# Performance work log

Measured on AMD Instinct MI355X. Metric: run time of the kernel, lower is better.

Reference implementation:

```python
import jax, jax.numpy as jnp
import numpy as np

NP_, NT_, NA_, NG_ = 50000, 200000, 20000, 500
ED, HID, H, C, L = 64, 64, 4, 16, 2
NEG_SLOPE = 0.2


def _edges(key, e, ns, nd):
    k1, k2 = jax.random.split(key)
    return jnp.stack([jax.random.randint(k1, (e,), 0, ns, dtype=jnp.int32),
                      jax.random.randint(k2, (e,), 0, nd, dtype=jnp.int32)])


def setup_inputs() -> dict:
    key = jax.random.key(0)
    ks = iter(jax.random.split(key, 64))
    nrm = lambda shp, s=0.1: (jax.random.normal(next(ks), shp, jnp.float32) * s)
    inp = {
        'playlist_x': nrm((NP_, 8), 1.0), 'track_x': nrm((NT_, 7), 1.0),
        'artist_x': nrm((NA_, 1), 1.0), 'genre_x': nrm((NG_, NG_), 1.0),
        'emb_playlist': nrm((NP_, ED)), 'emb_artist': nrm((NA_, ED)),
        'pf_W': nrm((8, ED)), 'pf_b': jnp.zeros((ED,)),
        'tf_W': nrm((7, ED)), 'tf_b': jnp.zeros((ED,)),
        'af_W': nrm((1, ED)), 'af_b': jnp.zeros((ED,)),
        'gf_W': nrm((NG_, ED)), 'gf_b': jnp.zeros((ED,)),
        'ip_W_playlist': nrm((2 * ED, HID)), 'ip_b_playlist': jnp.zeros((HID,)),
        'ip_W_track': nrm((ED, HID)), 'ip_b_track': jnp.zeros((HID,)),
        'ip_W_artist': nrm((2 * ED, HID)), 'ip_b_artist': jnp.zeros((HID,)),
        'ip_W_genre': nrm((ED, HID)), 'ip_b_genre': jnp.zeros((HID,)),
        # 8 relations x L layers, shared lin per relation (PyG GATConv with int in_channels)
        'gat_W': nrm((L, 8, HID, H * C)), 'gat_b': jnp.zeros((L, 8, H * C)),
        'gat_as': nrm((L, 8, H, C)), 'gat_ad': nrm((L, 8, H, C)),
        'ln_w': jnp.ones((L, HID)), 'ln_b': jnp.zeros((L, HID)),
        'op_W_playlist': nrm((HID, ED)), 'op_b_playlist': jnp.zeros((ED,)),
        'op_W_track': nrm((HID, ED)), 'op_b_track': jnp.zeros((ED,)),
        'op_W_artist': nrm((HID, ED)), 'op_b_artist': jnp.zeros((ED,)),
        'op_W_genre': nrm((HID, ED)), 'op_b_genre': jnp.zeros((ED,)),
        'playlist_idx': jnp.arange(NP_, dtype=jnp.int32),
        'artist_idx': jnp.arange(NA_, dtype=jnp.int32),
        'ei_contains': _edges(next(ks), 1000000, NP_, NT_),
        'ei_in_playlist': _edges(next(ks), 1000000, NT_, NP_),
        'ei_by': _edges(next(ks), 200000, NT_, NA_),
        'ei_created': _edges(next(ks), 200000, NA_, NT_),
        'ei_has_genre': _edges(next(ks), 600000, NT_, NG_),
        'ei_includes': _edges(next(ks), 600000, NG_, NT_),
        'ei_performs': _edges(next(ks), 60000, NA_, NG_),
        'ei_performed_by': _edges(next(ks), 60000, NG_, NA_),
    }
    return inp


def _gat(x_src, x_dst, ei, W, b, a_s, a_d, n_dst):
    # PyG GATConv: shared lin, edge softmax over dst, scatter-add aggregation
    hs = (x_src @ W).reshape(x_src.shape[0], H, C)
    hd = (x_dst @ W).reshape(x_dst.shape[0], H, C)
    es, ed = ei[0], ei[1]
    al_s = jnp.einsum('nhc,hc->nh', hs, a_s)  # [Ns,H]
    al_d = jnp.einsum('nhc,hc->nh', hd, a_d)  # [Nd,H]
    alpha = jax.nn.leaky_relu(al_s[es] + al_d[ed], NEG_SLOPE)  # [E,H]
    amax = jax.ops.segment_max(alpha, ed, num_segments=n_dst)
    amax = jnp.where(jnp.isfinite(amax), amax, 0.0)
    ex = jnp.exp(alpha - amax[ed])
    den = jax.ops.segment_sum(ex, ed, num_segments=n_dst)
    coef = ex / (den[ed] + 1e-16)
    msg = (hs[es] * coef[:, :, None]).reshape(es.shape[0], H * C)  # [E,H*C]
    return jax.ops.segment_sum(msg, ed, num_segments=n_dst) + b


def _ln(x, w, b):
    m = jnp.mean(x, -1, keepdims=True)
    v = jnp.mean((x - m) ** 2, -1, keepdims=True)
    return (x - m) * jax.lax.rsqrt(v + 1e-5) * w + b


def _forward(playlist_x, track_x, artist_x, genre_x, emb_playlist, emb_artist,
             pf_W, pf_b, tf_W, tf_b, af_W, af_b, gf_W, gf_b,
             ip_W_playlist, ip_b_playlist, ip_W_track, ip_b_track,
             ip_W_artist, ip_b_artist, ip_W_genre, ip_b_genre,
             gat_W, gat_b, gat_as, gat_ad, ln_w, ln_b,
             op_W_playlist, op_b_playlist, op_W_track, op_b_track,
             op_W_artist, op_b_artist, op_W_genre, op_b_genre,
             playlist_idx, artist_idx, ei_contains, ei_in_playlist, ei_by,
             ei_created, ei_has_genre, ei_includes, ei_performs, ei_performed_by):
    h_p = jnp.concatenate([emb_playlist[playlist_idx], playlist_x @ pf_W + pf_b], -1) @ ip_W_playlist + ip_b_playlist
    h_t = (track_x @ tf_W + tf_b) @ ip_W_track + ip_b_track
    h_a = jnp.concatenate([emb_artist[artist_idx], artist_x @ af_W + af_b], -1) @ ip_W_artist + ip_b_artist
    h_g = (genre_x @ gf_W + gf_b) @ ip_W_genre + ip_b_genre
    for i in range(L):
        pp, pt, pa, pg = h_p, h_t, h_a, h_g
        g = lambda r, xs, xd, ei, nd: _gat(xs, xd, ei, gat_W[i, r], gat_b[i, r], gat_as[i, r], gat_ad[i, r], nd)
        # relation index: 0 contains,1 in_playlist,2 by,3 created,4 has_genre,5 includes_track,6 performs_genre,7 performed_by
        nt = g(0, pp, pt, ei_contains, NT_) + g(3, pa, pt, ei_created, NT_) + g(5, pg, pt, ei_includes, NT_)
        np2 = g(1, pt, pp, ei_in_playlist, NP_)
        na = g(2, pt, pa, ei_by, NA_) + g(7, pg, pa, ei_performed_by, NA_)
        ng = g(4, pt, pg, ei_has_genre, NG_) + g(6, pa, pg, ei_performs, NG_)
        h_p, h_t, h_a, h_g = jax.nn.relu(np2), jax.nn.relu(nt), jax.nn.relu(na), jax.nn.relu(ng)
        if i > 0:  # residual only after first layer (matches `if i > 0`)
            h_p, h_t, h_a, h_g = h_p + pp, h_t + pt, h_a + pa, h_g + pg
        h_p, h_t, h_a, h_g = (_ln(v, ln_w[i], ln_b[i]) for v in (h_p, h_t, h_a, h_g))
    return jnp.concatenate([
        h_p @ op_W_playlist + op_b_playlist,
        h_t @ op_W_track + op_b_track,
        h_a @ op_W_artist + op_b_artist,
        h_g @ op_W_genre + op_b_genre], axis=0)  # [NP+NT+NA+NG, 64]


def reference(playlist_x, track_x, artist_x, genre_x, emb_playlist, emb_artist,
              pf_W, pf_b, tf_W, tf_b, af_W, af_b, gf_W, gf_b,
              ip_W_playlist, ip_b_playlist, ip_W_track, ip_b_track,
              ip_W_artist, ip_b_artist, ip_W_genre, ip_b_genre,
              gat_W, gat_b, gat_as, gat_ad, ln_w, ln_b,
              op_W_playlist, op_b_playlist, op_W_track, op_b_track,
              op_W_artist, op_b_artist, op_W_genre, op_b_genre,
              playlist_idx, artist_idx, ei_contains, ei_in_playlist, ei_by,
              ei_created, ei_has_genre, ei_includes, ei_performs, ei_performed_by):
    return _forward(playlist_x, track_x, artist_x, genre_x, emb_playlist, emb_artist,
                    pf_W, pf_b, tf_W, tf_b, af_W, af_b, gf_W, gf_b,
                    ip_W_playlist, ip_b_playlist, ip_W_track, ip_b_track,
                    ip_W_artist, ip_b_artist, ip_W_genre, ip_b_genre,
                    gat_W, gat_b, gat_as, gat_ad, ln_w, ln_b,
                    op_W_playlist, op_b_playlist, op_W_track, op_b_track,
                    op_W_artist, op_b_artist, op_W_genre, op_b_genre,
                    playlist_idx, artist_idx, ei_contains, ei_in_playlist, ei_by,
                    ei_created, ei_has_genre, ei_includes, ei_performs, ei_performed_by)
```

## Files before the change

### kernel.cpp

```cpp
#include <hip/hip_runtime.h>
#include <cstdint>

constexpr int NP=50000, NT=200000, NA=20000, NG=500;
constexpr int NTOT = NP+NT+NA+NG;
constexpr int RO_P=0, RO_T=NP, RO_A=NP+NT, RO_G=NP+NT+NA;
constexpr int E_TOT = 3720000;

constexpr int H_E [8] = {1000000,1000000,200000,200000,600000,600000,60000,60000};
constexpr int H_ES[9] = {0,1000000,2000000,2200000,2400000,3000000,3600000,3660000,3720000};
constexpr int H_NS[8] = {NP,NT,NT,NA,NT,NG,NA,NG};
constexpr int H_ND[8] = {NT,NP,NA,NT,NG,NT,NG,NA};
constexpr int H_SO[8] = {RO_P,RO_T,RO_T,RO_A,RO_T,RO_G,RO_A,RO_G};
constexpr int H_DO[8] = {RO_T,RO_P,RO_A,RO_T,RO_G,RO_T,RO_G,RO_A};
constexpr int H_RPO[8]= {0,200001,250002,270003,470004,470505,670506,671007};
constexpr int H_CO[8] = {0,200000,250000,270000,470000,470500,670500,671000};

__constant__ int c_E [8] = {1000000,1000000,200000,200000,600000,600000,60000,60000};
__constant__ int c_ES[9] = {0,1000000,2000000,2200000,2400000,3000000,3600000,3660000,3720000};
__constant__ int c_ND[8] = {200000,50000,20000,200000,500,200000,500,20000};
__constant__ int c_RPO[8]= {0,200001,250002,270003,470004,470505,670506,671007};
__constant__ int c_CO[8] = {0,200000,250000,270000,470000,470500,670500,671000};

__constant__ int sb_pref[9] = {0,196,245,265,461,462,658,659,679};
constexpr int SB_BLOCKS = 679;

constexpr int WSZ = 16384;
__constant__ int c_G [8] = {8,8,2,2,5,5,1,1};
__constant__ int c_CS[8] = {125000,125000,100000,100000,120000,120000,60000,60000};
__constant__ int c_NW[8] = {13,4,2,13,1,13,1,2};
__constant__ int gw_pref[9] = {0,104,136,140,166,171,236,237,239};
constexpr int GW_BLOCKS = 239;
__constant__ int c_C2[8] = {0,1600000,2000000,2040000,2440000,2442500,3442500,3443000};

constexpr int OWT=0;
constexpr int OBT=448;
constexpr int OWPX=512;
constexpr int OBP=1024;
constexpr int OAV=1088;
constexpr int OBA=1152;
constexpr int OBG=1216;
constexpr int OBAGG=1280;
constexpr int OWAS=1792;
constexpr int OWAD=5888;
constexpr int OWG=9984;

struct EiPtrs { const int* p[8]; };

__global__ __launch_bounds__(256) void k_prep(
  const float* __restrict__ pf_W, const float* __restrict__ pf_b,
  const float* __restrict__ tf_W, const float* __restrict__ tf_b,
  const float* __restrict__ af_W, const float* __restrict__ af_b,
  const float* __restrict__ gf_W, const float* __restrict__ gf_b,
  const float* __restrict__ ipWp, const float* __restrict__ ipbp,
  const float* __restrict__ ipWt, const float* __restrict__ ipbt,
  const float* __restrict__ ipWa, const float* __restrict__ ipba,
  const float* __restrict__ ipWg, const float* __restrict__ ipbg,
  const float* __restrict__ gatW, const float* __restrict__ gatB,
  const float* __restrict__ gatAs, const float* __restrict__ gatAd,
  float* __restrict__ cb)
{
  int tid = blockIdx.x*256 + threadIdx.x;
  int STR = gridDim.x*256;
  for(int i=tid;i<7*64;i+=STR){ int j=i>>6,c=i&63; float s=0.f;
    for(int k=0;k<64;k++) s += tf_W[j*64+k]*ipWt[k*64+c];
    cb[OWT+i]=s; }
  for(int i=tid;i<64;i+=STR){ float s=ipbt[i];
    for(int k=0;k<64;k++) s += tf_b[k]*ipWt[k*64+i];
    cb[OBT+i]=s; }
  for(int i=tid;i<8*64;i+=STR){ int j=i>>6,c=i&63; float s=0.f;
    for(int k=0;k<64;k++) s += pf_W[j*64+k]*ipWp[(64+k)*64+c];
    cb[OWPX+i]=s; }
  for(int i=tid;i<64;i+=STR){ float s=ipbp[i];
    for(int k=0;k<64;k++) s += pf_b[k]*ipWp[(64+k)*64+i];
    cb[OBP+i]=s; }
  for(int i=tid;i<64;i+=STR){ float s=0.f;
    for(int k=0;k<64;k++) s += af_W[k]*ipWa[(64+k)*64+i];
    cb[OAV+i]=s; }
  for(int i=tid;i<64;i+=STR){ float s=ipba[i];
    for(int k=0;k<64;k++) s += af_b[k]*ipWa[(64+k)*64+i];
    cb[OBA+i]=s; }
  for(int i=tid;i<64;i+=STR){ float s=ipbg[i];
    for(int k=0;k<64;k++) s += gf_b[k]*ipWg[k*64+i];
    cb[OBG+i]=s; }
  for(int i=tid;i<512;i+=STR){ int l=i>>8, t=(i>>6)&3, c=i&63;
    const float* B = gatB + l*8*64; float s;
    if(t==0)      s = B[1*64+c];
    else if(t==1) s = B[0*64+c]+B[3*64+c]+B[5*64+c];
    else if(t==2) s = B[2*64+c]+B[7*64+c];
    else          s = B[4*64+c]+B[6*64+c];
    cb[OBAGG+i]=s; }
  for(int i=tid;i<2*8*64*4;i+=STR){ int h=i&3, k=(i>>2)&63, lr=i>>8;
    const float* as = gatAs + lr*64;
    cb[OWAS+i] = ((k>>4)==h) ? as[h*16 + (k&15)] : 0.f;
    const float* W  = gatW + (size_t)lr*4096;
    const float* ad = gatAd + lr*64 + h*16;
    float d=0.f;
    for(int c=0;c<16;c++){ d += W[k*64+h*16+c]*ad[c]; }
    cb[OWAD+i]=d; }
  for(int i=tid;i<512*64;i+=STR){ int g=i>>6,c=i&63; float s=0.f;
    if(g<500){ for(int k=0;k<64;k++) s += gf_W[g*64+k]*ipWg[k*64+c]; }
    cb[OWG+i]=s; }
}

#define MM_DECL  __shared__ float sX[64*65]; __shared__ float sW[64*68]; \
  int tid=threadIdx.x; int rt=(tid>>4)<<2, ct=(tid&15)<<2; float acc[4][4];

#define MM_LOOP() \
  _Pragma("unroll 8") \
  for(int k=0;k<64;k++){ \
    float4 wv = *(const float4*)&sW[k*68+ct]; \
    float x0=sX[(rt+0)*65+k], x1=sX[(rt+1)*65+k], x2=sX[(rt+2)*65+k], x3=sX[(rt+3)*65+k]; \
    acc[0][0]+=x0*wv.x; acc[0][1]+=x0*wv.y; acc[0][2]+=x0*wv.z; acc[0][3]+=x0*wv.w; \
    acc[1][0]+=x1*wv.x; acc[1][1]+=x1*wv.y; acc[1][2]+=x1*wv.z; acc[1][3]+=x1*wv.w; \
    acc[2][0]+=x2*wv.x; acc[2][1]+=x2*wv.y; acc[2][2]+=x2*wv.z; acc[2][3]+=x2*wv.w; \
    acc[3][0]+=x3*wv.x; acc[3][1]+=x3*wv.y; acc[3][2]+=x3*wv.z; acc[3][3]+=x3*wv.w; \
  }

template<bool ALS>
__global__ __launch_bounds__(256) void k_mm64(const float* __restrict__ X, const float* __restrict__ W,
  const float* __restrict__ bias, float* __restrict__ Y, float* __restrict__ alsY,
  const float* __restrict__ was, int N)
{
  MM_DECL
  int row0 = blockIdx.x*64;
  for(int i=tid;i<4096;i+=256){
    int r=i>>6, k=i&63;
    sX[r*65+k] = (row0+r<N)? X[(size_t)(row0+r)*64+k] : 0.f;
    sW[r*68+k] = W[i];
  }
  __syncthreads();
  #pragma unroll
  for(int i=0;i<4;i++){ acc[i][0]=0.f;acc[i][1]=0.f;acc[i][2]=0.f;acc[i][3]=0.f; }
  MM_LOOP()
  float4 bv = make_float4(0.f,0.f,0.f,0.f);
  if(bias) bv = *(const float4*)&bias[ct];
  #pragma unroll
  for(int i=0;i<4;i++){
    int row=row0+rt+i;
    if(row<N) *(float4*)&Y[(size_t)row*64+ct] =
      make_float4(acc[i][0]+bv.x, acc[i][1]+bv.y, acc[i][2]+bv.z, acc[i][3]+bv.w);
  }
  if(ALS){
    float4 w0 = *(const float4*)&was[(ct+0)*4];
    float4 w1 = *(const float4*)&was[(ct+1)*4];
    float4 w2 = *(const float4*)&was[(ct+2)*4];
    float4 w3 = *(const float4*)&was[(ct+3)*4];
    #pragma unroll
    for(int i=0;i<4;i++){
      float4 p;
      p.x = acc[i][0]*w0.x + acc[i][1]*w1.x + acc[i][2]*w2.x + acc[i][3]*w3.x;
      p.y = acc[i][0]*w0.y + acc[i][1]*w1.y + acc[i][2]*w2.y + acc[i][3]*w3.y;
      p.z = acc[i][0]*w0.z + acc[i][1]*w1.z + acc[i][2]*w2.z + acc[i][3]*w3.z;
      p.w = acc[i][0]*w0.w + acc[i][1]*w1.w + acc[i][2]*w2.w + acc[i][3]*w3.w;
      #pragma unroll
      for(int m=1;m<16;m<<=1){
        p.x+=__shfl_xor(p.x,m); p.y+=__shfl_xor(p.y,m);
        p.z+=__shfl_xor(p.z,m); p.w+=__shfl_xor(p.w,m);
      }
      int row=row0+rt+i;
      if((tid&15)==0 && row<N) *(float4*)&alsY[(size_t)row*4] = p;
    }
  }
}

constexpr int BP=(NP+63)/64, BT=(NT+63)/64, BA=(NA+63)/64;
__global__ __launch_bounds__(256) void k_init(
  const float* __restrict__ px, const float* __restrict__ tx, const float* __restrict__ ax,
  const float* __restrict__ embp, const float* __restrict__ emba,
  const int* __restrict__ pidx, const int* __restrict__ aidx,
  const float* __restrict__ ipWp, const float* __restrict__ ipWa,
  const float* __restrict__ cb, float* __restrict__ hout)
{
  MM_DECL
  __shared__ float sE[64*9];
  int bid = blockIdx.x;
  if(bid < BP){
    int row0 = bid*64;
    for(int i=tid;i<4096;i+=256){
      int r=i>>6,k=i&63; int row=row0+r;
      sX[r*65+k] = (row<NP)? embp[(size_t)pidx[row]*64+k] : 0.f;
      sW[r*68+k] = ipWp[i];
    }
    for(int i=tid;i<512;i+=256){ int r=i>>3,j=i&7; int row=row0+r;
      sE[r*9+j] = (row<NP)? px[(size_t)row*8+j] : 0.f; }
    __syncthreads();
    { float4 b = *(const float4*)&cb[OBP+ct];
      #pragma unroll
      for(int i=0;i<4;i++){ acc[i][0]=b.x;acc[i][1]=b.y;acc[i][2]=b.z;acc[i][3]=b.w; } }
    #pragma unroll
    for(int j=0;j<8;j++){
      float4 w = *(const float4*)&cb[OWPX + j*64 + ct];
      #pragma unroll
      for(int i=0;i<4;i++){ float xe = sE[(rt+i)*9+j];
        acc[i][0]+=xe*w.x; acc[i][1]+=xe*w.y; acc[i][2]+=xe*w.z; acc[i][3]+=xe*w.w; }
    }
    MM_LOOP()
    #pragma unroll
    for(int i=0;i<4;i++){ int row=row0+rt+i;
      if(row<NP) *(float4*)&hout[(size_t)(RO_P+row)*64+ct] =
        make_float4(acc[i][0],acc[i][1],acc[i][2],acc[i][3]); }
  } else if(bid < BP+BT){
    int row0 = (bid-BP)*64;
    for(int i=tid;i<512;i+=256){ int r=i>>3,j=i&7; int row=row0+r;
      sE[r*9+j] = (row<NT && j<7)? tx[(size_t)row*7+j] : 0.f; }
    __syncthreads();
    { float4 b = *(const float4*)&cb[OBT+ct];
      #pragma unroll
      for(int i=0;i<4;i++){ acc[i][0]=b.x;acc[i][1]=b.y;acc[i][2]=b.z;acc[i][3]=b.w; } }
    #pragma unroll
    for(int j=0;j<7;j++){
      float4 w = *(const float4*)&cb[OWT + j*64 + ct];
      #pragma unroll
      for(int i=0;i<4;i++){ float xe = sE[(rt+i)*9+j];
        acc[i][0]+=xe*w.x; acc[i][1]+=xe*w.y; acc[i][2]+=xe*w.z; acc[i][3]+=xe*w.w; }
    }
    #pragma unroll
    for(int i=0;i<4;i++){ int row=row0+rt+i;
      if(row<NT) *(float4*)&hout[(size_t)(RO_T+row)*64+ct] =
        make_float4(acc[i][0],acc[i][1],acc[i][2],acc[i][3]); }
  } else {
    int row0 = (bid-BP-BT)*64;
    for(int i=tid;i<4096;i+=256){
      int r=i>>6,k=i&63; int row=row0+r;
      sX[r*65+k] = (row<NA)? emba[(size_t)aidx[row]*64+k] : 0.f;
      sW[r*68+k] = ipWa[i];
    }
    for(int i=tid;i<64;i+=256){ int row=row0+i; sE[i] = (row<NA)? ax[row] : 0.f; }
    __syncthreads();
    #pragma unroll
    for(int i=0;i<4;i++){
      float4 b = *(const float4*)&cb[OBA+ct];
      float4 av = *(const float4*)&cb[OAV+ct];
      float xe = sE[rt+i];
      acc[i][0]=b.x+xe*av.x; acc[i][1]=b.y+xe*av.y; acc[i][2]=b.z+xe*av.z; acc[i][3]=b.w+xe*av.w;
    }
    MM_LOOP()
    #pragma unroll
    for(int i=0;i<4;i++){ int row=row0+rt+i;
      if(row<NA) *(float4*)&hout[(size_t)(RO_A+row)*64+ct] =
        make_float4(acc[i][0],acc[i][1],acc[i][2],acc[i][3]); }
  }
}

__global__ __launch_bounds__(256) void k_init_g(const float* __restrict__ gx,
  const float* __restrict__ cb, float* __restrict__ hout)
{
  int wid = (blockIdx.x<<2)|(threadIdx.x>>6);
  int lane = threadIdx.x&63;
  if(wid>=NG) return;
  float acc = cb[OBG+lane];
  const float* WG = cb+OWG;
  for(int kb=0;kb<512;kb+=64){
    int k = kb+lane;
    float xv = (k<500)? gx[(size_t)wid*500+k] : 0.f;
    for(int j=0;j<64;j++){
      float x = __shfl(xv, j);
      acc += x * WG[(size_t)(kb+j)*64+lane];
    }
  }
  hout[(size_t)(RO_G+wid)*64+lane] = acc;
}

__global__ __launch_bounds__(1024) void k_cnt2(EiPtrs ei, int* __restrict__ cnt2){
  __shared__ int wcnt[WSZ];
  int bid=blockIdx.x, tid=threadIdx.x;
  int r=0;
  #pragma unroll
  for(int q=1;q<8;q++) if(bid>=gw_pref[q]) r=q;
  int local = bid - gw_pref[r];
  int NW=c_NW[r];
  int g = local/NW, w = local-g*NW;
  int lo=w*WSZ, nd=c_ND[r], n=min(WSZ,nd-lo);
  for(int i=tid;i<n;i+=1024) wcnt[i]=0;
  __syncthreads();
  int E=c_E[r], CS=c_CS[r];
  int e0=g*CS, e1=min(e0+CS,E);
  const int* __restrict__ pd = ei.p[r]+E;
  for(int e=e0+tid;e<e1;e+=1024){
    int d = pd[e]-lo;
    if((unsigned)d < (unsigned)n) atomicAdd(&wcnt[d],1);
  }
  __syncthreads();
  int* c = cnt2 + c_C2[r] + g*nd + lo;
  for(int i=tid;i<n;i+=1024) c[i]=wcnt[i];
}

__global__ __launch_bounds__(1024) void k_scan1(const int* __restrict__ cnt2, int* __restrict__ bsum){
  int bid = blockIdx.x;
  int r=0;
  #pragma unroll
  for(int q=1;q<8;q++) if(bid>=sb_pref[q]) r=q;
  int lb = bid - sb_pref[r];
  int nd = c_ND[r];
  int idx = lb*1024 + threadIdx.x;
  int v = 0;
  if(idx<nd){
    int G=c_G[r]; int base=c_C2[r]+idx;
    for(int g=0;g<G;g++) v += cnt2[base+g*nd];
  }
  #pragma unroll
  for(int m=1;m<64;m<<=1) v += __shfl_xor(v,m);
  __shared__ int wsum[16];
  int lane = threadIdx.x&63, wid=threadIdx.x>>6;
  if(lane==0) wsum[wid]=v;
  __syncthreads();
  if(threadIdx.x==0){
    int s=0;
    #pragma unroll
    for(int w=0;w<16;w++) s+=wsum[w];
    bsum[bid]=s;
  }
}

__global__ __launch_bounds__(256) void k_scan2(int* __restrict__ bsum, int* __restrict__ rowptr){
  int r = blockIdx.x;
  int nb = sb_pref[r+1]-sb_pref[r];
  __shared__ int s[200];
  int tid=threadIdx.x;
  if(tid<nb) s[tid]=bsum[sb_pref[r]+tid];
  __syncthreads();
  if(tid==0){
    int run=0;
    for(int i=0;i<nb;i++){ int t=s[i]; s[i]=run; run+=t; }
    rowptr[c_RPO[r]+c_ND[r]] = run;
  }
  __syncthreads();
  if(tid<nb) bsum[sb_pref[r]+tid]=s[tid];
}

__global__ __launch_bounds__(1024) void k_scan3(const int* __restrict__ cnt2, const int* __restrict__ bsum,
  int* __restrict__ rowptr){
  int bid = blockIdx.x;
  int r=0;
  #pragma unroll
  for(int q=1;q<8;q++) if(bid>=sb_pref[q]) r=q;
  int lb = bid - sb_pref[r];
  int nd = c_ND[r];
  int tid = threadIdx.x;
  int idx = lb*1024 + tid;
  int v = 0;
  if(idx<nd){
    int G=c_G[r]; int base=c_C2[r]+idx;
    for(int g=0;g<G;g++) v += cnt2[base+g*nd];
  }
  __shared__ int s[1024];
  s[tid]=v;
  __syncthreads();
  #pragma unroll
  for(int off=1;off<1024;off<<=1){
    int t = (tid>=off)? s[tid-off] : 0;
    __syncthreads();
    s[tid]+=t;
    __syncthreads();
  }
  int ex = s[tid]-v + bsum[bid];
  if(idx<nd) rowptr[c_RPO[r]+idx]=ex;
}

__global__ __launch_bounds__(1024) void k_off2(const int* __restrict__ rowptr, int* __restrict__ cnt2){
  int bid = blockIdx.x;
  int r=0;
  #pragma unroll
  for(int q=1;q<8;q++) if(bid>=sb_pref[q]) r=q;
  int idx = (bid-sb_pref[r])*1024 + threadIdx.x;
  int nd = c_ND[r];
  if(idx<nd){
    int run = rowptr[c_RPO[r]+idx];
    int G=c_G[r]; int base=c_C2[r]+idx;
    for(int g=0;g<G;g++){
      int t = cnt2[base+g*nd];
      cnt2[base+g*nd] = run;
      run += t;
    }
  }
}

__global__ __launch_bounds__(1024) void k_scat2(EiPtrs ei, const int* __restrict__ off2,
  int* __restrict__ col){
  __shared__ int wcur[WSZ];
  int bid=blockIdx.x, tid=threadIdx.x;
  int r=0;
  #pragma unroll
  for(int q=1;q<8;q++) if(bid>=gw_pref[q]) r=q;
  int local = bid - gw_pref[r];
  int NW=c_NW[r];
  int g = local/NW, w = local-g*NW;
  int lo=w*WSZ, nd=c_ND[r], n=min(WSZ,nd-lo);
  const int* o = off2 + c_C2[r] + g*nd + lo;
  for(int i=tid;i<n;i+=1024) wcur[i]=o[i];
  __syncthreads();
  int E=c_E[r], CS=c_CS[r];
  int e0=g*CS, e1=min(e0+CS,E);
  const int* __restrict__ ps = ei.p[r];
  const int* __restrict__ pd = ps+E;
  int* cl = col + c_ES[r];
  for(int e=e0+tid;e<e1;e+=1024){
    int d = pd[e]-lo;
    if((unsigned)d < (unsigned)n){
      int pos = atomicAdd(&wcur[d],1);
      cl[pos] = ps[e];
    }
  }
}

template<bool FIRST>
__global__ __launch_bounds__(256) void k_agg(const int* __restrict__ rp, const int* __restrict__ col,
  const float* __restrict__ hs, const float* __restrict__ als,
  const float* __restrict__ Xd, const float* __restrict__ wad,
  float* __restrict__ out, int nd)
{
  int wid = (blockIdx.x<<2)|(threadIdx.x>>6);
  int lane = threadIdx.x&63;
  if(wid>=nd) return;
  float x = Xd[(size_t)wid*64+lane];
  float4 wv = *(const float4*)&wad[lane*4];
  float a0=x*wv.x, a1=x*wv.y, a2=x*wv.z, a3=x*wv.w;
  #pragma unroll
  for(int m=1;m<64;m<<=1){
    a0+=__shfl_xor(a0,m); a1+=__shfl_xor(a1,m); a2+=__shfl_xor(a2,m); a3+=__shfl_xor(a3,m);
  }
  int h = lane>>4;
  float adv = (h==0)?a0:(h==1)?a1:(h==2)?a2:a3;
  int start = rp[wid], end = rp[wid+1];
  float den=0.f, acc=0.f;
  int j = start;
  for(; j+4<=end; j+=4){
    int s0=col[j], s1=col[j+1], s2=col[j+2], s3=col[j+3];
    float A0=als[(size_t)s0*4+h], A1=als[(size_t)s1*4+h];
    float A2=als[(size_t)s2*4+h], A3=als[(size_t)s3*4+h];
    float h0=hs[(size_t)s0*64+lane], h1=hs[(size_t)s1*64+lane];
    float h2=hs[(size_t)s2*64+lane], h3=hs[(size_t)s3*64+lane];
    float v0=A0+adv; v0=fmaxf(v0,0.2f*v0); float e0=__expf(v0);
    float v1=A1+adv; v1=fmaxf(v1,0.2f*v1); float e1=__expf(v1);
    float v2=A2+adv; v2=fmaxf(v2,0.2f*v2); float e2=__expf(v2);
    float v3=A3+adv; v3=fmaxf(v3,0.2f*v3); float e3=__expf(v3);
    den+=e0; acc+=e0*h0;
    den+=e1; acc+=e1*h1;
    den+=e2; acc+=e2*h2;
    den+=e3; acc+=e3*h3;
  }
  for(; j<end; j++){
    int s = col[j];
    float ah = als[(size_t)s*4+h] + adv;
    ah = fmaxf(ah, 0.2f*ah);
    float e = __expf(ah);
    den += e;
    acc += e*hs[(size_t)s*64+lane];
  }
  float r = acc/(den+1e-16f);
  if(FIRST) out[(size_t)wid*64+lane] = r;
  else      out[(size_t)wid*64+lane] += r;
}

template<bool FIRST>
__global__ __launch_bounds__(1024) void k_agg_blk(const int* __restrict__ rp, const int* __restrict__ col,
  const float* __restrict__ hs, const float* __restrict__ als,
  const float* __restrict__ Xd, const float* __restrict__ wad,
  float* __restrict__ out, int nd)
{
  int d = blockIdx.x;
  if(d>=nd) return;
  int tid=threadIdx.x, lane=tid&63, wid=tid>>6;
  __shared__ float sden[16*4];
  __shared__ float sacc[16][64];
  float x = Xd[(size_t)d*64+lane];
  float4 wv = *(const float4*)&wad[lane*4];
  float a0=x*wv.x, a1=x*wv.y, a2=x*wv.z, a3=x*wv.w;
  #pragma unroll
  for(int m=1;m<64;m<<=1){
    a0+=__shfl_xor(a0,m); a1+=__shfl_xor(a1,m); a2+=__shfl_xor(a2,m); a3+=__shfl_xor(a3,m);
  }
  int h = lane>>4;
  float adv = (h==0)?a0:(h==1)?a1:(h==2)?a2:a3;
  int start = rp[d], end = rp[d+1];
  float den=0.f, acc=0.f;
  for(int j=start+wid;j<end;j+=16){
    int s = col[j];
    float ah = als[(size_t)s*4+h] + adv;
    ah = fmaxf(ah, 0.2f*ah);
    float e = __expf(ah);
    den += e;
    acc += e*hs[(size_t)s*64+lane];
  }
  if((lane&15)==0) sden[wid*4+h]=den;
  sacc[wid][lane]=acc;
  __syncthreads();
  if(tid<64){
    float s=0.f, dt=0.f;
    #pragma unroll
    for(int w=0;w<16;w++){ s+=sacc[w][tid]; dt+=sden[w*4+(tid>>4)]; }
    float r = s/(dt+1e-16f);
    if(FIRST) out[(size_t)d*64+tid] = r;
    else      out[(size_t)d*64+tid] += r;
  }
}

__global__ __launch_bounds__(256) void k_post(float* __restrict__ hnew, const float* __restrict__ hold,
  const float* __restrict__ bagg, const float* __restrict__ lnw, const float* __restrict__ lnb, int layer)
{
  int wid = (blockIdx.x<<2)|(threadIdx.x>>6);
  int lane = threadIdx.x&63;
  if(wid>=NTOT) return;
  int t = (wid<RO_T)?0 : (wid<RO_A)?1 : (wid<RO_G)?2 : 3;
  size_t idx = (size_t)wid*64+lane;
  float v = hnew[idx] + bagg[t*64+lane];
  v = fmaxf(v, 0.f);
  if(layer) v += hold[idx];
  float s = v;
  #pragma unroll
  for(int m=1;m<64;m<<=1) s += __shfl_xor(s,m);
  float mu = s*(1.f/64.f);
  float d = v-mu;
  float q = d*d;
  #pragma unroll
  for(int m=1;m<64;m<<=1) q += __shfl_xor(q,m);
  float var = q*(1.f/64.f);
  hnew[idx] = d*rsqrtf(var+1e-5f)*lnw[lane] + lnb[lane];
}

extern "C" void kernel_launch(void* const* d_in, const int* in_sizes, int n_in,
                              void* d_out, int out_size, void* d_ws, size_t ws_size,
                              hipStream_t stream)
{
  const float* playlist_x=(const float*)d_in[0];
  const float* track_x   =(const float*)d_in[1];
  const float* artist_x  =(const float*)d_in[2];
  const float* genre_x   =(const float*)d_in[3];
  const float* embp=(const float*)d_in[4];
  const float* emba=(const float*)d_in[5];
  const float* pf_W=(const float*)d_in[6];  const float* pf_b=(const float*)d_in[7];
  const float* tf_W=(const float*)d_in[8];  const float* tf_b=(const float*)d_in[9];
  const float* af_W=(const float*)d_in[10]; const float* af_b=(const float*)d_in[11];
  const float* gf_W=(const float*)d_in[12]; const float* gf_b=(const float*)d_in[13];
  const float* ipWp=(const float*)d_in[14]; const float* ipbp=(const float*)d_in[15];
  const float* ipWt=(const float*)d_in[16]; const float* ipbt=(const float*)d_in[17];
  const float* ipWa=(const float*)d_in[18]; const float* ipba=(const float*)d_in[19];
  const float* ipWg=(const float*)d_in[20]; const float* ipbg=(const float*)d_in[21];
  const float* gatW=(const float*)d_in[22]; const float* gatB=(const float*)d_in[23];
  const float* gatAs=(const float*)d_in[24];const float* gatAd=(const float*)d_in[25];
  const float* lnw=(const float*)d_in[26];  const float* lnb=(const float*)d_in[27];
  const float* opWp=(const float*)d_in[28]; const float* opbp=(const float*)d_in[29];
  const float* opWt=(const float*)d_in[30]; const float* opbt=(const float*)d_in[31];
  const float* opWa=(const float*)d_in[32]; const float* opba=(const float*)d_in[33];
  const float* opWg=(const float*)d_in[34]; const float* opbg=(const float*)d_in[35];
  const int* pidx=(const int*)d_in[36];
  const int* aidx=(const int*)d_in[37];
  EiPtrs ei;
  for(int r=0;r<8;r++) ei.p[r]=(const int*)d_in[38+r];

  char* ws=(char*)d_ws;
  float* cb = (float*)ws;
  size_t o_hB  = 256*1024;
  float* hB = (float*)(ws+o_hB);
  size_t o_hs  = o_hB  + (size_t)NTOT*64*4;
  float* hs = (float*)(ws+o_hs);
  size_t o_als = o_hs  + (size_t)NT*64*4;
  float* als=(float*)(ws+o_als);
  size_t o_rp  = o_als + (size_t)NT*4*4 + (size_t)NT*4*4;
  int* rowptr=(int*)(ws+o_rp);
  size_t o_col = o_rp  + 691008*4;
  int* col=(int*)(ws+o_col);
  int* cnt2=(int*)(ws+o_hs);
  int* bsum=cnt2+3463000;
  float* hA=(float*)d_out;

  k_prep<<<128,256,0,stream>>>(pf_W,pf_b,tf_W,tf_b,af_W,af_b,gf_W,gf_b,
      ipWp,ipbp,ipWt,ipbt,ipWa,ipba,ipWg,ipbg,gatW,gatB,gatAs,gatAd,cb);
  k_init<<<BP+BT+BA,256,0,stream>>>(playlist_x,track_x,artist_x,embp,emba,pidx,aidx,ipWp,ipWa,cb,hA);
  k_init_g<<<(NG+3)/4,256,0,stream>>>(genre_x,cb,hA);

  k_cnt2<<<GW_BLOCKS,1024,0,stream>>>(ei,cnt2);
  k_scan1<<<SB_BLOCKS,1024,0,stream>>>(cnt2,bsum);
  k_scan2<<<8,256,0,stream>>>(bsum,rowptr);
  k_scan3<<<SB_BLOCKS,1024,0,stream>>>(cnt2,bsum,rowptr);
  k_off2<<<SB_BLOCKS,1024,0,stream>>>(rowptr,cnt2);
  k_scat2<<<GW_BLOCKS,1024,0,stream>>>(ei,cnt2,col);

  for(int l=0;l<2;l++){
    float* hcur = l? hB : hA;
    float* hnew = l? hA : hB;
    for(int r=0;r<8;r++){
      int Ns=H_NS[r], Nd=H_ND[r];
      const float* Xs = hcur + (size_t)H_SO[r]*64;
      const float* Xd = hcur + (size_t)H_DO[r]*64;
      const float* W  = gatW + (size_t)(l*8+r)*4096;
      const float* was = cb+OWAS+(size_t)(l*8+r)*256;
      const float* wad = cb+OWAD+(size_t)(l*8+r)*256;
      float* outp = hnew + (size_t)H_DO[r]*64;
      bool first = (r==0)||(r==1)||(r==2)||(r==4);
      k_mm64<true><<<(Ns+63)/64,256,0,stream>>>(Xs,W,nullptr,hs,als,was,Ns);
      if(r==4 || r==6){
        if(first) k_agg_blk<true ><<<Nd,1024,0,stream>>>(rowptr+H_RPO[r], col+H_ES[r], hs, als, Xd, wad, outp, Nd);
        else      k_agg_blk<false><<<Nd,1024,0,stream>>>(rowptr+H_RPO[r], col+H_ES[r], hs, als, Xd, wad, outp, Nd);
      } else {
        if(first) k_agg<true ><<<(Nd+3)/4,256,0,stream>>>(rowptr+H_RPO[r], col+H_ES[r], hs, als, Xd, wad, outp, Nd);
        else      k_agg<false><<<(Nd+3)/4,256,0,stream>>>(rowptr+H_RPO[r], col+H_ES[r], hs, als, Xd, wad, outp, Nd);
      }
    }
    k_post<<<(NTOT+3)/4,256,0,stream>>>(hnew, hcur, cb+OBAGG+l*256, lnw+l*64, lnb+l*64, l);
  }
  k_mm64<false><<<(NP+63)/64,256,0,stream>>>(hA+(size_t)RO_P*64, opWp, opbp, hA+(size_t)RO_P*64, nullptr, nullptr, NP);
  k_mm64<false><<<(NT+63)/64,256,0,stream>>>(hA+(size_t)RO_T*64, opWt, opbt, hA+(size_t)RO_T*64, nullptr, nullptr, NT);
  k_mm64<false><<<(NA+63)/64,256,0,stream>>>(hA+(size_t)RO_A*64, opWa, opba, hA+(size_t)RO_A*64, nullptr, nullptr, NA);
  k_mm64<false><<<(NG+63)/64,256,0,stream>>>(hA+(size_t)RO_G*64, opWg, opbg, hA+(size_t)RO_G*64, nullptr, nullptr, NG);
}
```

Before: 1.642 ms.

## Double CSR build grid granularity and deepen gather unrolling in aggregation kernels

Doubles the number of edge chunks per relation in the count/scatter CSR-building kernels, halving chunk size and enlarging the per-chunk count buffer and bsum offset. The warp-per-node aggregation loop is unrolled by 8 instead of 4. The block-per-node kernel now handles four strided edges per iteration, so more independent gathers are in flight and memory latency is hidden better. The risks are more scan work over the larger count array and higher register pressure.

```diff
diff --git a/kernel.cpp b/kernel.cpp
--- a/kernel.cpp
+++ b/kernel.cpp
@@ -25,12 +25,12 @@
 constexpr int SB_BLOCKS = 679;
 
 constexpr int WSZ = 16384;
-__constant__ int c_G [8] = {8,8,2,2,5,5,1,1};
-__constant__ int c_CS[8] = {125000,125000,100000,100000,120000,120000,60000,60000};
+__constant__ int c_G [8] = {16,16,4,4,10,10,2,2};
+__constant__ int c_CS[8] = {62500,62500,50000,50000,60000,60000,30000,30000};
 __constant__ int c_NW[8] = {13,4,2,13,1,13,1,2};
-__constant__ int gw_pref[9] = {0,104,136,140,166,171,236,237,239};
-constexpr int GW_BLOCKS = 239;
-__constant__ int c_C2[8] = {0,1600000,2000000,2040000,2440000,2442500,3442500,3443000};
+__constant__ int gw_pref[9] = {0,208,272,280,332,342,472,474,478};
+constexpr int GW_BLOCKS = 478;
+__constant__ int c_C2[8] = {0,3200000,4000000,4080000,4880000,4885000,6885000,6886000};
 
 constexpr int OWT=0;
 constexpr int OBT=448;
@@ -424,8 +424,72 @@
   int start = rp[wid], end = rp[wid+1];
   float den=0.f, acc=0.f;
   int j = start;
-  for(; j+4<=end; j+=4){
-    int s0=col[j], s1=col[j+1], s2=col[j+2], s3=col[j+3];
+  for(; j+8<=end; j+=8){
+    int s0=col[j],   s1=col[j+1], s2=col[j+2], s3=col[j+3];
+    int s4=col[j+4], s5=col[j+5], s6=col[j+6], s7=col[j+7];
+    float A0=als[(size_t)s0*4+h], A1=als[(size_t)s1*4+h];
+    float A2=als[(size_t)s2*4+h], A3=als[(size_t)s3*4+h];
+    float A4=als[(size_t)s4*4+h], A5=als[(size_t)s5*4+h];
+    float A6=als[(size_t)s6*4+h], A7=als[(size_t)s7*4+h];
+    float h0=hs[(size_t)s0*64+lane], h1=hs[(size_t)s1*64+lane];
+    float h2=hs[(size_t)s2*64+lane], h3=hs[(size_t)s3*64+lane];
+    float h4=hs[(size_t)s4*64+lane], h5=hs[(size_t)s5*64+lane];
+    float h6=hs[(size_t)s6*64+lane], h7=hs[(size_t)s7*64+lane];
+    float v0=A0+adv; v0=fmaxf(v0,0.2f*v0); float e0=__expf(v0);
+    float v1=A1+adv; v1=fmaxf(v1,0.2f*v1); float e1=__expf(v1);
+    float v2=A2+adv; v2=fmaxf(v2,0.2f*v2); float e2=__expf(v2);
+    float v3=A3+adv; v3=fmaxf(v3,0.2f*v3); float e3=__expf(v3);
+    float v4=A4+adv; v4=fmaxf(v4,0.2f*v4); float e4=__expf(v4);
+    float v5=A5+adv; v5=fmaxf(v5,0.2f*v5); float e5=__expf(v5);
+    float v6=A6+adv; v6=fmaxf(v6,0.2f*v6); float e6=__expf(v6);
+    float v7=A7+adv; v7=fmaxf(v7,0.2f*v7); float e7=__expf(v7);
+    den+=e0; acc+=e0*h0;
+    den+=e1; acc+=e1*h1;
+    den+=e2; acc+=e2*h2;
+    den+=e3; acc+=e3*h3;
+    den+=e4; acc+=e4*h4;
+    den+=e5; acc+=e5*h5;
+    den+=e6; acc+=e6*h6;
+    den+=e7; acc+=e7*h7;
+  }
+  for(; j<end; j++){
+    int s = col[j];
+    float ah = als[(size_t)s*4+h] + adv;
+    ah = fmaxf(ah, 0.2f*ah);
+    float e = __expf(ah);
+    den += e;
+    acc += e*hs[(size_t)s*64+lane];
+  }
+  float r = acc/(den+1e-16f);
+  if(FIRST) out[(size_t)wid*64+lane] = r;
+  else      out[(size_t)wid*64+lane] += r;
+}
+
+template<bool FIRST>
+__global__ __launch_bounds__(1024) void k_agg_blk(const int* __restrict__ rp, const int* __restrict__ col,
+  const float* __restrict__ hs, const float* __restrict__ als,
+  const float* __restrict__ Xd, const float* __restrict__ wad,
+  float* __restrict__ out, int nd)
+{
+  int d = blockIdx.x;
+  if(d>=nd) return;
+  int tid=threadIdx.x, lane=tid&63, wid=tid>>6;
+  __shared__ float sden[16*4];
+  __shared__ float sacc[16][64];
+  float x = Xd[(size_t)d*64+lane];
+  float4 wv = *(const float4*)&wad[lane*4];
+  float a0=x*wv.x, a1=x*wv.y, a2=x*wv.z, a3=x*wv.w;
+  #pragma unroll
+  for(int m=1;m<64;m<<=1){
+    a0+=__shfl_xor(a0,m); a1+=__shfl_xor(a1,m); a2+=__shfl_xor(a2,m); a3+=__shfl_xor(a3,m);
+  }
+  int h = lane>>4;
+  float adv = (h==0)?a0:(h==1)?a1:(h==2)?a2:a3;
+  int start = rp[d], end = rp[d+1];
+  float den=0.f, acc=0.f;
+  int j = start+wid;
+  for(; j+48<end; j+=64){
+    int s0=col[j], s1=col[j+16], s2=col[j+32], s3=col[j+48];
     float A0=als[(size_t)s0*4+h], A1=als[(size_t)s1*4+h];
     float A2=als[(size_t)s2*4+h], A3=als[(size_t)s3*4+h];
     float h0=hs[(size_t)s0*64+lane], h1=hs[(size_t)s1*64+lane];
@@ -439,42 +503,7 @@
     den+=e2; acc+=e2*h2;
     den+=e3; acc+=e3*h3;
   }
-  for(; j<end; j++){
-    int s = col[j];
-    float ah = als[(size_t)s*4+h] + adv;
-    ah = fmaxf(ah, 0.2f*ah);
-    float e = __expf(ah);
-    den += e;
-    acc += e*hs[(size_t)s*64+lane];
-  }
-  float r = acc/(den+1e-16f);
-  if(FIRST) out[(size_t)wid*64+lane] = r;
-  else      out[(size_t)wid*64+lane] += r;
-}
-
-template<bool FIRST>
-__global__ __launch_bounds__(1024) void k_agg_blk(const int* __restrict__ rp, const int* __restrict__ col,
-  const float* __restrict__ hs, const float* __restrict__ als,
-  const float* __restrict__ Xd, const float* __restrict__ wad,
-  float* __restrict__ out, int nd)
-{
-  int d = blockIdx.x;
-  if(d>=nd) return;
-  int tid=threadIdx.x, lane=tid&63, wid=tid>>6;
-  __shared__ float sden[16*4];
-  __shared__ float sacc[16][64];
-  float x = Xd[(size_t)d*64+lane];
-  float4 wv = *(const float4*)&wad[lane*4];
-  float a0=x*wv.x, a1=x*wv.y, a2=x*wv.z, a3=x*wv.w;
-  #pragma unroll
-  for(int m=1;m<64;m<<=1){
-    a0+=__shfl_xor(a0,m); a1+=__shfl_xor(a1,m); a2+=__shfl_xor(a2,m); a3+=__shfl_xor(a3,m);
-  }
-  int h = lane>>4;
-  float adv = (h==0)?a0:(h==1)?a1:(h==2)?a2:a3;
-  int start = rp[d], end = rp[d+1];
-  float den=0.f, acc=0.f;
-  for(int j=start+wid;j<end;j+=16){
+  for(; j<end; j+=16){
     int s = col[j];
     float ah = als[(size_t)s*4+h] + adv;
     ah = fmaxf(ah, 0.2f*ah);
@@ -561,7 +590,7 @@
   size_t o_col = o_rp  + 691008*4;
   int* col=(int*)(ws+o_col);
   int* cnt2=(int*)(ws+o_hs);
-  int* bsum=cnt2+3463000;
+  int* bsum=cnt2+6926000;
   float* hA=(float*)d_out;
 
   k_prep<<<128,256,0,stream>>>(pf_W,pf_b,tf_W,tf_b,af_W,af_b,gf_W,gf_b,
```

Result: no change. 1.643 ms (+0.1%).
